# Optimization experiments

Hardware: AMD Instinct MI355X
Metric: run time of the kernel (lower is better)

## Reference

```python
import jax, jax.numpy as jnp
import numpy as np

N, E1, E2, P, H = 4096, 131072, 131072, 65536, 128
ROLE_VOCAB, ROLE_DIM, IDX_VOCAB, IDX_DIM = 8, 16, 1024, 8


def _lin_init(key, fan_in, fan_out):
    k1, k2 = jax.random.split(key)
    bound = 1.0 / np.sqrt(fan_in)
    W = jax.random.uniform(k1, (fan_in, fan_out), jnp.float32, -bound, bound)
    b = jax.random.uniform(k2, (fan_out,), jnp.float32, -bound, bound)
    return W, b


def setup_inputs() -> dict:
    key = jax.random.key(0)
    ks = jax.random.split(key, 24)
    d = {}
    d["block_features"] = jax.random.normal(ks[0], (N, 16), jnp.float32)
    d["role_ids"] = jax.random.randint(ks[1], (N,), 0, ROLE_VOCAB)
    d["b2b_src"] = jax.random.randint(ks[2], (E1,), 0, N)
    d["b2b_dst"] = jax.random.randint(ks[3], (E1,), 0, N)
    d["b2b_w"] = jax.random.uniform(ks[4], (E1,), jnp.float32)
    d["p2b_pin"] = jax.random.randint(ks[5], (E2,), 0, P)
    d["p2b_block"] = jax.random.randint(ks[6], (E2,), 0, N)
    d["p2b_w"] = jax.random.uniform(ks[7], (E2,), jnp.float32)
    d["pins_pos"] = jax.random.normal(ks[8], (P, 2), jnp.float32)
    d["area_targets"] = jax.random.uniform(ks[9], (N,), jnp.float32)
    # parameters
    d["role_emb"] = jax.random.normal(ks[10], (ROLE_VOCAB, ROLE_DIM), jnp.float32)
    d["idx_emb"] = jax.random.normal(ks[11], (IDX_VOCAB, IDX_DIM), jnp.float32)
    d["in_W1"], d["in_b1"] = _lin_init(ks[12], 16 + IDX_DIM + ROLE_DIM, H)
    d["in_W2"], d["in_b2"] = _lin_init(ks[13], H, H)
    d["b2b_W1"], d["b2b_b1"] = _lin_init(ks[14], 2 * H + 1, H)
    d["b2b_W2"], d["b2b_b2"] = _lin_init(ks[15], H, H)
    d["p2b_W1"], d["p2b_b1"] = _lin_init(ks[16], H + 3, H)
    d["p2b_W2"], d["p2b_b2"] = _lin_init(ks[17], H, H)
    d["self_W"], d["self_b"] = _lin_init(ks[18], H, H)
    d["ln_g"] = jnp.ones((H,), jnp.float32)
    d["ln_b"] = jnp.zeros((H,), jnp.float32)
    d["gp_W1"], d["gp_b1"] = _lin_init(ks[19], 2 * H, H)
    d["gp_W2"], d["gp_b2"] = _lin_init(ks[20], H, H)
    return d


def _mlp2(x, W1, b1, W2, b2):
    return jax.nn.relu(x @ W1 + b1) @ W2 + b2


def _forward(block_features, role_ids, b2b_src, b2b_dst, b2b_w, p2b_pin, p2b_block,
             p2b_w, pins_pos, area_targets, role_emb, idx_emb, in_W1, in_b1, in_W2,
             in_b2, b2b_W1, b2b_b1, b2b_W2, b2b_b2, p2b_W1, p2b_b1, p2b_W2, p2b_b2,
             self_W, self_b, ln_g, ln_b, gp_W1, gp_b1, gp_W2, gp_b2):
    n = block_features.shape[0]
    role_e = role_emb[role_ids]                       # [N, role_dim]
    idx_e = idx_emb[jnp.arange(n) % IDX_VOCAB]        # [N, idx_dim]
    x = jnp.concatenate([block_features, role_e, idx_e], axis=-1)
    h = jax.nn.relu(_mlp2(x, in_W1, in_b1, in_W2, in_b2))  # input_proj ends in ReLU

    # --- b2b messages: two directed messages per undirected edge ---
    max_b2b = jax.lax.stop_gradient(jnp.maximum(jnp.max(jnp.abs(b2b_w)), 1.0))
    w = (b2b_w / max_b2b)[:, None]                    # [E1, 1]
    hi, hj = h[b2b_src], h[b2b_dst]                   # [E1, H]
    m_ij = _mlp2(jnp.concatenate([hi, hj, w], -1), b2b_W1, b2b_b1, b2b_W2, b2b_b2)
    m_ji = _mlp2(jnp.concatenate([hj, hi, w], -1), b2b_W1, b2b_b1, b2b_W2, b2b_b2)
    agg = jnp.zeros_like(h).at[b2b_src].add(m_ij).at[b2b_dst].add(m_ji)

    # --- p2b messages ---
    total_area = jnp.maximum(jnp.sum(area_targets), 1e-6)
    case_scale = jax.lax.stop_gradient(jnp.maximum(jnp.sqrt(total_area), 1e-6))
    max_p2b = jax.lax.stop_gradient(jnp.maximum(jnp.max(jnp.abs(p2b_w)), 1.0))
    pin_feats = jnp.concatenate(
        [pins_pos[p2b_pin] / case_scale, (p2b_w / max_p2b)[:, None]], axis=-1)  # [E2, 3]
    m_p = _mlp2(jnp.concatenate([h[p2b_block], pin_feats], -1),
                p2b_W1, p2b_b1, p2b_W2, p2b_b2)
    agg = agg.at[p2b_block].add(m_p)

    # --- combine + LayerNorm ---
    z = h @ self_W + self_b + agg
    mu = jnp.mean(z, axis=-1, keepdims=True)
    var = jnp.mean(jnp.square(z - mu), axis=-1, keepdims=True)
    block_embeddings = (z - mu) / jnp.sqrt(var + 1e-5) * ln_g + ln_b

    pooled = jnp.concatenate(
        [block_embeddings.mean(axis=0), block_embeddings.max(axis=0)], axis=-1)
    graph_embedding = _mlp2(pooled, gp_W1, gp_b1, gp_W2, gp_b2)
    return block_embeddings, graph_embedding


def reference(block_features, role_ids, b2b_src, b2b_dst, b2b_w, p2b_pin, p2b_block,
              p2b_w, pins_pos, area_targets, role_emb, idx_emb, in_W1, in_b1, in_W2,
              in_b2, b2b_W1, b2b_b1, b2b_W2, b2b_b2, p2b_W1, p2b_b1, p2b_W2, p2b_b2,
              self_W, self_b, ln_g, ln_b, gp_W1, gp_b1, gp_W2, gp_b2):
    block_embeddings, graph_embedding = _forward(
        block_features, role_ids, b2b_src, b2b_dst, b2b_w, p2b_pin, p2b_block,
        p2b_w, pins_pos, area_targets, role_emb, idx_emb, in_W1, in_b1, in_W2,
        in_b2, b2b_W1, b2b_b1, b2b_W2, b2b_b2, p2b_W1, p2b_b1, p2b_W2, p2b_b2,
        self_W, self_b, ln_g, ln_b, gp_W1, gp_b1, gp_W2, gp_b2)
    block_mask = jnp.ones((block_features.shape[0],), dtype=bool)
    return block_embeddings, graph_embedding, block_mask
```

## Files before the change

### kernel.cpp

```cpp
#include <hip/hip_runtime.h>
#include <hip/hip_bf16.h>

#define N_NODES 4096
#define HDIM    128
#define E1      131072
#define E2      131072
#define NMSG_B2B (2 * E1)
#define CAPB    192
#define CAPP    96

#define OFF_PSUM   8
#define OFF_PMAX   136
#define OFF_HB     264
#define OFF_P      (OFF_HB + 262144)
#define OFF_Q      (OFF_P + 524288)
#define OFF_R      (OFF_Q + 524288)
#define OFF_CP     (OFF_R + 524288)
#define OFF_B2H    (OFF_CP + 24576)
#define OFF_B2L    (OFF_B2H + 8192)
#define OFF_P2H    (OFF_B2L + 8192)
#define OFF_P2L    (OFF_P2H + 8192)
#define OFF_SWP    (OFF_P2L + 8192)
#define OFF_IW1    (OFF_SWP + 8192)
#define OFF_IW2    (OFF_IW1 + 4096)
#define OFF_WLAST  (OFF_IW2 + 8192)
#define OFF_PEXTRA (OFF_WLAST + 128)
#define OFF_CNTB   (OFF_PEXTRA + 384)
#define OFF_CNTP   (OFF_CNTB + 4096)
#define OFF_BKB    (OFF_CNTP + 4096)
#define OFF_BKP    (OFF_BKB + 2 * N_NODES * CAPB)
#define WS_FLOATS  (OFF_BKP + 2 * N_NODES * CAPP)

typedef short short8 __attribute__((ext_vector_type(8)));
typedef float f32x4 __attribute__((ext_vector_type(4)));

__device__ __forceinline__ unsigned short f2bf(float f) {
  union { float f; unsigned u; } v; v.f = f;
  unsigned r = v.u + 0x7fffu + ((v.u >> 16) & 1u);
  return (unsigned short)(r >> 16);
}
__device__ __forceinline__ float bf2f(unsigned short h) {
  return __uint_as_float((unsigned)h << 16);
}
__device__ __forceinline__ int il(int c) { return ((c & 63) << 1) | (c >> 6); }
__device__ __forceinline__ f32x4 relu4(f32x4 v) {
  f32x4 r;
  r[0] = fmaxf(v[0], 0.f); r[1] = fmaxf(v[1], 0.f);
  r[2] = fmaxf(v[2], 0.f); r[3] = fmaxf(v[3], 0.f);
  return r;
}

__global__ __launch_bounds__(256) void setup_kernel(const float* __restrict__ b2bw,
                                                    const float* __restrict__ p2bw,
                                                    const float* __restrict__ area,
                                                    const float* __restrict__ bW1,
                                                    const float* __restrict__ bW2,
                                                    const float* __restrict__ pW1,
                                                    const float* __restrict__ pW2,
                                                    const float* __restrict__ sWm,
                                                    const float* __restrict__ iW1,
                                                    const float* __restrict__ iW2,
                                                    float* __restrict__ ws) {
  __shared__ float red[256];
  int b = blockIdx.x, t = threadIdx.x;
  if (b < 32) {
    float m = 0.f;
    for (int i = b * 256 + t; i < E1; i += 32 * 256) m = fmaxf(m, fabsf(b2bw[i]));
    red[t] = m; __syncthreads();
    for (int s = 128; s > 0; s >>= 1) { if (t < s) red[t] = fmaxf(red[t], red[t + s]); __syncthreads(); }
    if (t == 0) atomicMax((unsigned*)&ws[0], __float_as_uint(red[0]));
  } else if (b < 64) {
    float m = 0.f;
    for (int i = (b - 32) * 256 + t; i < E2; i += 32 * 256) m = fmaxf(m, fabsf(p2bw[i]));
    red[t] = m; __syncthreads();
    for (int s = 128; s > 0; s >>= 1) { if (t < s) red[t] = fmaxf(red[t], red[t + s]); __syncthreads(); }
    if (t == 0) atomicMax((unsigned*)&ws[1], __float_as_uint(red[0]));
  } else if (b < 96) {
    float s0 = 0.f;
    for (int i = (b - 64) * 256 + t; i < N_NODES; i += 32 * 256) s0 += area[i];
    red[t] = s0; __syncthreads();
    for (int s = 128; s > 0; s >>= 1) { if (t < s) red[t] += red[t + s]; __syncthreads(); }
    if (t == 0) atomicAdd(&ws[2], red[0]);
  } else if (b == 96) {
    if (t < HDIM) ((int*)ws)[OFF_PMAX + t] = 0x80000000;
    int* cB = (int*)ws + OFF_CNTB;
    for (int i = t; i < 2 * N_NODES; i += 256) cB[i] = 0;
  } else {
    unsigned short* Cp  = (unsigned short*)(ws + OFF_CP);
    unsigned short* B2h = (unsigned short*)(ws + OFF_B2H);
    unsigned short* B2l = (unsigned short*)(ws + OFF_B2L);
    unsigned short* P2h = (unsigned short*)(ws + OFF_P2H);
    unsigned short* P2l = (unsigned short*)(ws + OFF_P2L);
    unsigned short* Swp = (unsigned short*)(ws + OFF_SWP);
    unsigned short* I1p = (unsigned short*)(ws + OFF_IW1);
    unsigned short* I2p = (unsigned short*)(ws + OFF_IW2);
    float* wlast = ws + OFF_WLAST;
    float* pextra = ws + OFF_PEXTRA;
    const int total = 156160;
    for (int x = (b - 97) * 256 + t; x < total; x += 128 * 256) {
      if (x < 49152) {
        int j = x & 7, lane = (x >> 3) & 63, ks = (x >> 9) & 3, nc = x >> 11;
        int col = nc * 16 + (lane & 15), k = ks * 32 + (lane >> 4) * 8 + j;
        float v;
        if (col < 128)      v = bW1[k * 128 + col];
        else if (col < 256) v = bW1[(128 + k) * 128 + (col - 128)];
        else                v = pW1[k * 128 + (col - 256)];
        Cp[x] = f2bf(v);
      } else if (x < 114688) {
        int u = (x - 49152) & 16383, which = (x - 49152) >> 14;
        int j = u & 7, lane = (u >> 3) & 63, ks = (u >> 9) & 3, nt = u >> 11;
        int n = nt * 16 + (lane & 15), k = ks * 32 + (lane >> 4) * 8 + j;
        float v = (which < 2) ? bW2[k * 128 + n] : pW2[k * 128 + n];
        unsigned short hi = f2bf(v);
        unsigned short outv = (which & 1) ? f2bf(v - bf2f(hi)) : hi;
        ((which < 2) ? ((which & 1) ? B2l : B2h) : ((which & 1) ? P2l : P2h))[u] = outv;
      } else if (x < 131072) {
        int u = x - 114688;
        int j = u & 7, lane = (u >> 3) & 63, ks = (u >> 9) & 3, nt = u >> 11;
        int n = nt * 16 + (lane & 15), k = ks * 32 + (lane >> 4) * 8 + j;
        Swp[u] = f2bf(sWm[k * 128 + n]);
      } else if (x < 139264) {
        int u = x - 131072;
        int j = u & 7, lane = (u >> 3) & 63, ks = (u >> 9) & 1, nt = u >> 10;
        int n = nt * 16 + (lane & 15), k = ks * 32 + (lane >> 4) * 8 + j;
        I1p[u] = (k < 40) ? f2bf(iW1[k * 128 + n]) : 0;
      } else if (x < 155648) {
        int u = x - 139264;
        int j = u & 7, lane = (u >> 3) & 63, ks = (u >> 9) & 3, nt = u >> 11;
        int n = nt * 16 + (lane & 15), k = ks * 32 + (lane >> 4) * 8 + j;
        I2p[u] = f2bf(iW2[k * 128 + n]);
      } else if (x < 155776) {
        int c = x - 155648;
        wlast[il(c)] = bW1[256 * 128 + c];
      } else {
        int u = x - 155776;
        int r = u >> 7, c = u & 127;
        pextra[r * 128 + il(c)] = pW1[(128 + r) * 128 + c];
      }
    }
  }
}

__global__ __launch_bounds__(512) void mid_kernel(const int* __restrict__ src,
                                                  const int* __restrict__ dst,
                                                  const int* __restrict__ pblk,
                                                  const int* __restrict__ ppin,
                                                  const float* __restrict__ bwv,
                                                  const float* __restrict__ pwv,
                                                  const float* __restrict__ pins,
                                                  const float* __restrict__ bfeat,
                                                  const int* __restrict__ rid,
                                                  const float* __restrict__ remb,
                                                  const float* __restrict__ iemb,
                                                  const float* __restrict__ ib1,
                                                  const float* __restrict__ ib2,
                                                  const float* __restrict__ bb1,
                                                  const float* __restrict__ pb1,
                                                  float* __restrict__ ws,
                                                  unsigned short* __restrict__ hb) {
  __shared__ __attribute__((aligned(16))) unsigned short xs[16 * 72];
  __shared__ __attribute__((aligned(16))) unsigned short h1s[16 * 136];
  __shared__ __attribute__((aligned(16))) unsigned short hs[16 * 136];
  int tid = threadIdx.x;
  if (blockIdx.x < 768) {
    int i = blockIdx.x * 512 + tid;
    int* cntB = (int*)ws + OFF_CNTB;
    int* cntP = (int*)ws + OFF_CNTP;
    uint2* BKB = (uint2*)((int*)ws + OFF_BKB);
    uint2* BKP = (uint2*)((int*)ws + OFF_BKP);
    if (i < NMSG_B2B) {
      int e = i >> 1, d = i & 1;
      int tg = d ? dst[e] : src[e];
      int o  = d ? src[e] : dst[e];
      int pos = atomicAdd(&cntB[tg], 1);
      if (pos < CAPB) {
        uint2 v; v.x = (unsigned)o; v.y = __float_as_uint(bwv[e]);
        BKB[tg * CAPB + pos] = v;
      }
    } else {
      int e = i - NMSG_B2B;
      int pin = ppin[e];
      int tg = pblk[e];
      int pos = atomicAdd(&cntP[tg], 1);
      if (pos < CAPP) {
        uint2 v;
        v.x = ((unsigned)f2bf(pins[pin * 2 + 1]) << 16) | (unsigned)f2bf(pins[pin * 2]);
        v.y = __float_as_uint(pwv[e]);
        BKP[tg * CAPP + pos] = v;
      }
    }
    return;
  }
  const unsigned short* I1p = (const unsigned short*)(ws + OFF_IW1);
  const unsigned short* I2p = (const unsigned short*)(ws + OFF_IW2);
  const unsigned short* Cp  = (const unsigned short*)(ws + OFF_CP);
  float* P = ws + OFF_P;
  float* Q = ws + OFF_Q;
  float* R = ws + OFF_R;
  int n0 = (blockIdx.x - 768) * 16;
  for (int idx = tid; idx < 1024; idx += 512) {
    int m = idx >> 6, c = idx & 63;
    int n = n0 + m;
    float v = 0.f;
    if (c < 16)      v = bfeat[n * 16 + c];
    else if (c < 32) v = remb[rid[n] * 16 + (c - 16)];
    else if (c < 40) v = iemb[(n & 1023) * 8 + (c - 32)];
    xs[m * 72 + c] = f2bf(v);
  }
  __syncthreads();
  int lane = tid & 63, wv = tid >> 6;
  int l15 = lane & 15, q = lane >> 4;
  f32x4 zero = {0.f, 0.f, 0.f, 0.f};
  f32x4 a1 = zero;
#pragma unroll
  for (int ks = 0; ks < 2; ks++) {
    short8 af = *(const short8*)(&xs[l15 * 72 + ks * 32 + q * 8]);
    short8 bfr = *(const short8*)(I1p + ((wv * 2 + ks) * 64 + lane) * 8);
    a1 = __builtin_amdgcn_mfma_f32_16x16x32_bf16(af, bfr, a1, 0, 0, 0);
  }
  {
    int n = wv * 16 + l15;
    float b = ib1[n];
#pragma unroll
    for (int r = 0; r < 4; r++)
      h1s[(q * 4 + r) * 136 + n] = f2bf(fmaxf(a1[r] + b, 0.f));
  }
  __syncthreads();
  f32x4 a2 = zero;
#pragma unroll
  for (int ks = 0; ks < 4; ks++) {
    short8 af = *(const short8*)(&h1s[l15 * 136 + ks * 32 + q * 8]);
    short8 bfr = *(const short8*)(I2p + ((wv * 4 + ks) * 64 + lane) * 8);
    a2 = __builtin_amdgcn_mfma_f32_16x16x32_bf16(af, bfr, a2, 0, 0, 0);
  }
  {
    int n = wv * 16 + l15;
    float b = ib2[n];
#pragma unroll
    for (int r = 0; r < 4; r++) {
      unsigned short hv = f2bf(fmaxf(a2[r] + b, 0.f));
      hs[(q * 4 + r) * 136 + n] = hv;
      hb[(n0 + q * 4 + r) * 128 + n] = hv;
    }
  }
  __syncthreads();
  f32x4 a3[3];
#pragma unroll
  for (int i = 0; i < 3; i++) a3[i] = zero;
#pragma unroll
  for (int ks = 0; ks < 4; ks++) {
    short8 af = *(const short8*)(&hs[l15 * 136 + ks * 32 + q * 8]);
#pragma unroll
    for (int j = 0; j < 3; j++) {
      short8 bfr = *(const short8*)(Cp + (((3 * wv + j) * 4 + ks) * 64 + lane) * 8);
      a3[j] = __builtin_amdgcn_mfma_f32_16x16x32_bf16(af, bfr, a3[j], 0, 0, 0);
    }
  }
#pragma unroll
  for (int j = 0; j < 3; j++) {
    int col = (3 * wv + j) * 16 + l15;
    int arr = col >> 7, cc = col & 127;
    float bias = (arr == 0) ? bb1[cc] : ((arr == 2) ? pb1[cc] : 0.f);
    float* dstp = (arr == 0) ? P : ((arr == 1) ? Q : R);
    int ic = il(cc);
#pragma unroll
    for (int r = 0; r < 4; r++)
      dstp[(n0 + q * 4 + r) * 128 + ic] = a3[j][r] + bias;
  }
}

__global__ __launch_bounds__(1024) void fused_kernel(const unsigned short* __restrict__ hb,
                                                     const float* __restrict__ sb,
                                                     const float* __restrict__ lng,
                                                     const float* __restrict__ lnb,
                                                     const float* __restrict__ bb2,
                                                     const float* __restrict__ pb2,
                                                     const float* __restrict__ gW1,
                                                     const float* __restrict__ gb1,
                                                     const float* __restrict__ gW2,
                                                     const float* __restrict__ gb2,
                                                     float* __restrict__ ws,
                                                     float* __restrict__ out) {
  __shared__ __attribute__((aligned(16))) unsigned short A[16 * 648];
  __shared__ float zp[2][16 * 128];
  __shared__ float zs[16 * 133];
  __shared__ float muS[16], rsg[16];
  __shared__ float partS[16][16], partQ[16][16];
  __shared__ float psumL[8][128];
  __shared__ int   pmaxL[8][128];
  __shared__ int   isLast;
  int tid = threadIdx.x;
  int n0 = blockIdx.x * 16;
  int lane = tid & 63, wv = tid >> 6;
  const int* cntBp = (const int*)ws + OFF_CNTB;
  const int* cntPp = (const int*)ws + OFF_CNTP;
  if (tid < 256) {
    int m = tid >> 4, o = (tid & 15) * 8;
    *(uint4*)(&A[m * 648 + o]) = *(const uint4*)(hb + (n0 + m) * 128 + o);
  }
  {
    const uint2* BKB = (const uint2*)((const int*)ws + OFF_BKB);
    const uint2* BKP = (const uint2*)((const int*)ws + OFF_BKP);
    const float* Pm = ws + OFF_P;
    const float* Qm = ws + OFF_Q;
    const float* Rm = ws + OFF_R;
    float invb = 1.f / fmaxf(__uint_as_float(((const unsigned*)ws)[0]), 1.f);
    float invp = 1.f / fmaxf(__uint_as_float(((const unsigned*)ws)[1]), 1.f);
    float cs = fmaxf(sqrtf(fmaxf(ws[2], 1e-6f)), 1e-6f);
    float invc = 1.f / cs;
    int l5 = lane & 31, hf = lane >> 5;
    f32x4 wl = *(const f32x4*)(ws + OFF_WLAST + 4 * l5);
    f32x4 e0 = *(const f32x4*)(ws + OFF_PEXTRA + 4 * l5);
    f32x4 e1 = *(const f32x4*)(ws + OFF_PEXTRA + 128 + 4 * l5);
    f32x4 e2 = *(const f32x4*)(ws + OFF_PEXTRA + 256 + 4 * l5);
    wl *= invb; e0 *= invc; e1 *= invc; e2 *= invp;
    int ln = wv;
    int node = n0 + ln;
    {
      int cnt = min(cntBp[node], CAPB);
      const uint2* bk = BKB + node * CAPB;
      f32x4 p4 = *(const f32x4*)(Pm + node * 128 + 4 * l5);
      f32x4 acc = {0.f, 0.f, 0.f, 0.f};
      int m = 0;
      if (cnt >= 8) {
        uint2 k0 = bk[hf], k1 = bk[2 + hf], k2 = bk[4 + hf], k3 = bk[6 + hf];
        while (m + 16 <= cnt) {
          uint2 t0 = bk[m + 8 + hf],  t1 = bk[m + 10 + hf];
          uint2 t2 = bk[m + 12 + hf], t3 = bk[m + 14 + hf];
          f32x4 q0 = *(const f32x4*)(Qm + k0.x * 128 + 4 * l5);
          f32x4 q1 = *(const f32x4*)(Qm + k1.x * 128 + 4 * l5);
          f32x4 q2 = *(const f32x4*)(Qm + k2.x * 128 + 4 * l5);
          f32x4 q3 = *(const f32x4*)(Qm + k3.x * 128 + 4 * l5);
          acc += relu4(p4 + __uint_as_float(k0.y) * wl + q0);
          acc += relu4(p4 + __uint_as_float(k1.y) * wl + q1);
          acc += relu4(p4 + __uint_as_float(k2.y) * wl + q2);
          acc += relu4(p4 + __uint_as_float(k3.y) * wl + q3);
          k0 = t0; k1 = t1; k2 = t2; k3 = t3;
          m += 8;
        }
        f32x4 q0 = *(const f32x4*)(Qm + k0.x * 128 + 4 * l5);
        f32x4 q1 = *(const f32x4*)(Qm + k1.x * 128 + 4 * l5);
        f32x4 q2 = *(const f32x4*)(Qm + k2.x * 128 + 4 * l5);
        f32x4 q3 = *(const f32x4*)(Qm + k3.x * 128 + 4 * l5);
        acc += relu4(p4 + __uint_as_float(k0.y) * wl + q0);
        acc += relu4(p4 + __uint_as_float(k1.y) * wl + q1);
        acc += relu4(p4 + __uint_as_float(k2.y) * wl + q2);
        acc += relu4(p4 + __uint_as_float(k3.y) * wl + q3);
        m += 8;
      }
      for (; m + 2 <= cnt; m += 2) {
        uint2 k = bk[m + hf];
        f32x4 q = *(const f32x4*)(Qm + k.x * 128 + 4 * l5);
        acc += relu4(p4 + __uint_as_float(k.y) * wl + q);
      }
      if (m < cnt) {
        uint2 k = bk[m + hf];
        f32x4 q = *(const f32x4*)(Qm + (k.x & (N_NODES - 1)) * 128 + 4 * l5);
        f32x4 v = relu4(p4 + __uint_as_float(k.y) * wl + q);
        if (hf == 0) acc += v;
      }
      f32x4 tot;
#pragma unroll
      for (int j = 0; j < 4; j++) tot[j] = acc[j] + __shfl_xor(acc[j], 32, 64);
      if (hf == 0) {
        unsigned short h0 = f2bf(tot[0]), h1 = f2bf(tot[1]);
        unsigned short h2 = f2bf(tot[2]), h3 = f2bf(tot[3]);
        *(unsigned*)(&A[ln * 648 + 128 + 2 * l5])      = (unsigned)h0 | ((unsigned)h2 << 16);
        *(unsigned*)(&A[ln * 648 + 128 + 64 + 2 * l5]) = (unsigned)h1 | ((unsigned)h3 << 16);
        unsigned short g0 = f2bf(tot[0] - bf2f(h0)), g1 = f2bf(tot[1] - bf2f(h1));
        unsigned short g2 = f2bf(tot[2] - bf2f(h2)), g3 = f2bf(tot[3] - bf2f(h3));
        *(unsigned*)(&A[ln * 648 + 256 + 2 * l5])      = (unsigned)g0 | ((unsigned)g2 << 16);
        *(unsigned*)(&A[ln * 648 + 256 + 64 + 2 * l5]) = (unsigned)g1 | ((unsigned)g3 << 16);
      }
    }
    {
      int cnt = min(cntPp[node], CAPP);
      const uint2* bk = BKP + node * CAPP;
      f32x4 r4 = *(const f32x4*)(Rm + node * 128 + 4 * l5);
      f32x4 acc = {0.f, 0.f, 0.f, 0.f};
      int m = 0;
      for (; m + 4 <= cnt; m += 4) {
        uint2 ka = bk[m + hf], kb = bk[m + 2 + hf];
        float a0 = __uint_as_float((ka.x & 0xFFFFu) << 16);
        float a1 = __uint_as_float(ka.x & 0xFFFF0000u);
        float a2 = __uint_as_float(ka.y);
        float b0 = __uint_as_float((kb.x & 0xFFFFu) << 16);
        float b1 = __uint_as_float(kb.x & 0xFFFF0000u);
        float b2 = __uint_as_float(kb.y);
        acc += relu4(r4 + a0 * e0 + a1 * e1 + a2 * e2);
        acc += relu4(r4 + b0 * e0 + b1 * e1 + b2 * e2);
      }
      for (; m + 2 <= cnt; m += 2) {
        uint2 ka = bk[m + hf];
        float a0 = __uint_as_float((ka.x & 0xFFFFu) << 16);
        float a1 = __uint_as_float(ka.x & 0xFFFF0000u);
        float a2 = __uint_as_float(ka.y);
        acc += relu4(r4 + a0 * e0 + a1 * e1 + a2 * e2);
      }
      if (m < cnt) {
        uint2 ka = bk[m + hf];
        float a0 = __uint_as_float((ka.x & 0xFFFFu) << 16);
        float a1 = __uint_as_float(ka.x & 0xFFFF0000u);
        float a2 = __uint_as_float(ka.y);
        f32x4 v = relu4(r4 + a0 * e0 + a1 * e1 + a2 * e2);
        if (hf == 0) acc += v;
      }
      f32x4 tot;
#pragma unroll
      for (int j = 0; j < 4; j++) tot[j] = acc[j] + __shfl_xor(acc[j], 32, 64);
      if (hf == 0) {
        unsigned short h0 = f2bf(tot[0]), h1 = f2bf(tot[1]);
        unsigned short h2 = f2bf(tot[2]), h3 = f2bf(tot[3]);
        *(unsigned*)(&A[ln * 648 + 384 + 2 * l5])      = (unsigned)h0 | ((unsigned)h2 << 16);
        *(unsigned*)(&A[ln * 648 + 384 + 64 + 2 * l5]) = (unsigned)h1 | ((unsigned)h3 << 16);
        unsigned short g0 = f2bf(tot[0] - bf2f(h0)), g1 = f2bf(tot[1] - bf2f(h1));
        unsigned short g2 = f2bf(tot[2] - bf2f(h2)), g3 = f2bf(tot[3] - bf2f(h3));
        *(unsigned*)(&A[ln * 648 + 512 + 2 * l5])      = (unsigned)g0 | ((unsigned)g2 << 16);
        *(unsigned*)(&A[ln * 648 + 512 + 64 + 2 * l5]) = (unsigned)g1 | ((unsigned)g3 << 16);
      }
    }
  }
  __syncthreads();
  int l15 = lane & 15, q = lane >> 4;
  int ct = wv & 7, half = wv >> 3;
  f32x4 zero = {0.f, 0.f, 0.f, 0.f};
  f32x4 acc = zero;
  const unsigned short* bufs[7] = {
    (const unsigned short*)(ws + OFF_SWP), (const unsigned short*)(ws + OFF_B2H),
    (const unsigned short*)(ws + OFF_B2L), (const unsigned short*)(ws + OFF_B2H),
    (const unsigned short*)(ws + OFF_P2H), (const unsigned short*)(ws + OFF_P2L),
    (const unsigned short*)(ws + OFF_P2H)};
  const int segs[7] = {0, 128, 128, 256, 384, 384, 512};
  int p0 = half ? 4 : 0, p1 = half ? 7 : 4;
  for (int p = p0; p < p1; p++) {
#pragma unroll
    for (int ks = 0; ks < 4; ks++) {
      short8 af = *(const short8*)(&A[l15 * 648 + segs[p] + ks * 32 + q * 8]);
      short8 bfr = *(const short8*)(bufs[p] + ((ct * 4 + ks) * 64 + lane) * 8);
      acc = __builtin_amdgcn_mfma_f32_16x16x32_bf16(af, bfr, acc, 0, 0, 0);
    }
  }
  {
    int nn = ct * 16 + l15;
#pragma unroll
    for (int r = 0; r < 4; r++)
      zp[half][(q * 4 + r) * 128 + nn] = acc[r];
  }
  __syncthreads();
  {
    int idx = tid;
    for (int rep = 0; rep < 2; rep++, idx += 1024) {
      int row = idx >> 7, c = idx & 127;
      float cb = (float)cntBp[n0 + row], cp = (float)cntPp[n0 + row];
      zs[row * 133 + c] = zp[0][row * 128 + c] + zp[1][row * 128 + c]
                        + sb[c] + cb * bb2[c] + cp * pb2[c];
    }
  }
  __syncthreads();
  if (tid < 256) {
    int r = tid >> 4, g = tid & 15;
    const float* zr = &zs[r * 133 + g * 8];
    float s = 0.f, s2 = 0.f;
#pragma unroll
    for (int i = 0; i < 8; i++) { float v = zr[i]; s += v; s2 += v * v; }
    partS[r][g] = s; partQ[r][g] = s2;
  }
  __syncthreads();
  if (tid < 16) {
    float s = 0.f, s2 = 0.f;
#pragma unroll
    for (int g = 0; g < 16; g++) { s += partS[tid][g]; s2 += partQ[tid][g]; }
    float m = s * (1.f / 128.f);
    float var = s2 * (1.f / 128.f) - m * m;
    muS[tid] = m;
    rsg[tid] = rsqrtf(fmaxf(var, 0.f) + 1e-5f);
  }
  __syncthreads();
  {
    int c = tid & 127, grp = tid >> 7;
    float g = lng[c], b = lnb[c];
    float ls = 0.f; int lm = 0x80000000;
    for (int r = grp * 2; r < grp * 2 + 2; r++) {
      float v = (zs[r * 133 + c] - muS[r]) * rsg[r] * g + b;
      out[(n0 + r) * 128 + c] = v;
      ls += v;
      int e = __float_as_int(v);
      e = e >= 0 ? e : (e ^ 0x7fffffff);
      lm = max(lm, e);
    }
    psumL[grp][c] = ls; pmaxL[grp][c] = lm;
  }
  __syncthreads();
  if (tid < 128) {
    float s = 0.f; int mx = 0x80000000;
#pragma unroll
    for (int g = 0; g < 8; g++) { s += psumL[g][tid]; mx = max(mx, pmaxL[g][tid]); }
    atomicAdd(&ws[OFF_PSUM + tid], s);
    atomicMax(&((int*)ws)[OFF_PMAX + tid], mx);
  }
  if (tid < 16) out[N_NODES * HDIM + HDIM + n0 + tid] = 1.0f;
  __syncthreads();
  if (tid == 0) {
    __threadfence();
    int v = atomicAdd(&((int*)ws)[3], 1);
    isLast = (v == (int)gridDim.x - 1);
  }
  __syncthreads();
  if (!isLast) return;
  __shared__ float pooled[256];
  __shared__ float gpart[8][128];
  __shared__ float g1[128];
  if (tid < 128) {
    pooled[tid] = atomicAdd(&ws[OFF_PSUM + tid], 0.f) * (1.f / (float)N_NODES);
  } else if (tid < 256) {
    int e = atomicAdd(&((int*)ws)[OFF_PMAX + (tid - 128)], 0);
    int bits = e >= 0 ? e : (e ^ 0x7fffffff);
    pooled[tid] = __int_as_float(bits);
  }
  __syncthreads();
  {
    int c = tid & 127, g = tid >> 7;
    float acc2 = 0.f;
#pragma unroll 8
    for (int k = g * 32; k < g * 32 + 32; k++) acc2 += pooled[k] * gW1[k * 128 + c];
    gpart[g][c] = acc2;
  }
  __syncthreads();
  if (tid < 128) {
    float s = gb1[tid];
#pragma unroll
    for (int g = 0; g < 8; g++) s += gpart[g][tid];
    g1[tid] = fmaxf(s, 0.f);
  }
  __syncthreads();
  {
    int c = tid & 127, g = tid >> 7;
    float acc2 = 0.f;
#pragma unroll 8
    for (int k = g * 16; k < g * 16 + 16; k++) acc2 += g1[k] * gW2[k * 128 + c];
    gpart[g][c] = acc2;
  }
  __syncthreads();
  if (tid < 128) {
    float s = gb2[tid];
#pragma unroll
    for (int g = 0; g < 8; g++) s += gpart[g][tid];
    out[N_NODES * HDIM + tid] = s;
  }
}

extern "C" void kernel_launch(void* const* d_in, const int* in_sizes, int n_in,
                              void* d_out, int out_size, void* d_ws, size_t ws_size,
                              hipStream_t stream) {
  const float* bfeat = (const float*)d_in[0];
  const int*   rid   = (const int*)d_in[1];
  const int*   bsrc  = (const int*)d_in[2];
  const int*   bdst  = (const int*)d_in[3];
  const float* bw    = (const float*)d_in[4];
  const int*   ppin  = (const int*)d_in[5];
  const int*   pblk  = (const int*)d_in[6];
  const float* pw    = (const float*)d_in[7];
  const float* pins  = (const float*)d_in[8];
  const float* area  = (const float*)d_in[9];
  const float* remb  = (const float*)d_in[10];
  const float* iemb  = (const float*)d_in[11];
  const float* inW1  = (const float*)d_in[12];
  const float* inb1  = (const float*)d_in[13];
  const float* inW2  = (const float*)d_in[14];
  const float* inb2  = (const float*)d_in[15];
  const float* bW1   = (const float*)d_in[16];
  const float* bb1   = (const float*)d_in[17];
  const float* bW2   = (const float*)d_in[18];
  const float* bb2   = (const float*)d_in[19];
  const float* pW1   = (const float*)d_in[20];
  const float* pb1   = (const float*)d_in[21];
  const float* pW2   = (const float*)d_in[22];
  const float* pb2   = (const float*)d_in[23];
  const float* sW    = (const float*)d_in[24];
  const float* sb    = (const float*)d_in[25];
  const float* lng   = (const float*)d_in[26];
  const float* lnb   = (const float*)d_in[27];
  const float* gW1   = (const float*)d_in[28];
  const float* gb1   = (const float*)d_in[29];
  const float* gW2   = (const float*)d_in[30];
  const float* gb2   = (const float*)d_in[31];

  float* ws  = (float*)d_ws;
  float* out = (float*)d_out;
  unsigned short* hb = (unsigned short*)(ws + OFF_HB);

  hipMemsetAsync(d_ws, 0, 264 * sizeof(float), stream);
  setup_kernel<<<225, 256, 0, stream>>>(bw, pw, area,
                                        bW1, bW2, pW1, pW2, sW, inW1, inW2, ws);
  mid_kernel<<<1024, 512, 0, stream>>>(bsrc, bdst, pblk, ppin, bw, pw, pins,
                                       bfeat, rid, remb, iemb, inb1, inb2, bb1, pb1,
                                       ws, hb);
  fused_kernel<<<256, 1024, 0, stream>>>(hb, sb, lng, lnb, bb2, pb2,
                                         gW1, gb1, gW2, gb2, ws, out);
}
```

Before: 191.0 us.

## Move edge bucketing into setup kernel and stage bucket entries in shared memory

The edge bucketing (atomic slot claim and write of edge records into per-node buckets) moves from mid_kernel into setup_kernel, so mid_kernel runs only the node MLP on 256 blocks. The fused kernel now copies the first STGB/STGP bucket entries per node into shared memory, reusing the z-buffer space through a union, and reads any overflow from global memory. The global atomic reductions for the weight maxima and the area sum become per-block partials that the fused kernel reduces with shuffles. This trades a larger setup launch and an extra staging pass for less global latency in the gather loops and fewer atomics.

```diff
diff --git a/kernel.cpp b/kernel.cpp
--- a/kernel.cpp
+++ b/kernel.cpp
@@ -8,10 +8,15 @@
 #define NMSG_B2B (2 * E1)
 #define CAPB    192
 #define CAPP    96
-
-#define OFF_PSUM   8
-#define OFF_PMAX   136
-#define OFF_HB     264
+#define STGB    96
+#define STGP    48
+
+#define OFF_CNTB   8
+#define OFF_CNTP   (OFF_CNTB + 4096)
+#define OFF_RED    (OFF_CNTP + 4096)
+#define OFF_PSUM   (OFF_RED + 96)
+#define OFF_PMAX   (OFF_PSUM + 128)
+#define OFF_HB     (OFF_PMAX + 128)
 #define OFF_P      (OFF_HB + 262144)
 #define OFF_Q      (OFF_P + 524288)
 #define OFF_R      (OFF_Q + 524288)
@@ -25,9 +30,7 @@
 #define OFF_IW2    (OFF_IW1 + 4096)
 #define OFF_WLAST  (OFF_IW2 + 8192)
 #define OFF_PEXTRA (OFF_WLAST + 128)
-#define OFF_CNTB   (OFF_PEXTRA + 384)
-#define OFF_CNTP   (OFF_CNTB + 4096)
-#define OFF_BKB    (OFF_CNTP + 4096)
+#define OFF_BKB    (OFF_PEXTRA + 384)
 #define OFF_BKP    (OFF_BKB + 2 * N_NODES * CAPB)
 #define WS_FLOATS  (OFF_BKP + 2 * N_NODES * CAPP)
 
@@ -60,6 +63,11 @@
                                                     const float* __restrict__ sWm,
                                                     const float* __restrict__ iW1,
                                                     const float* __restrict__ iW2,
+                                                    const int* __restrict__ src,
+                                                    const int* __restrict__ dst,
+                                                    const int* __restrict__ pblk,
+                                                    const int* __restrict__ ppin,
+                                                    const float* __restrict__ pins,
                                                     float* __restrict__ ws) {
   __shared__ float red[256];
   int b = blockIdx.x, t = threadIdx.x;
@@ -68,24 +76,25 @@
     for (int i = b * 256 + t; i < E1; i += 32 * 256) m = fmaxf(m, fabsf(b2bw[i]));
     red[t] = m; __syncthreads();
     for (int s = 128; s > 0; s >>= 1) { if (t < s) red[t] = fmaxf(red[t], red[t + s]); __syncthreads(); }
-    if (t == 0) atomicMax((unsigned*)&ws[0], __float_as_uint(red[0]));
+    if (t == 0) ws[OFF_RED + b] = red[0];
   } else if (b < 64) {
     float m = 0.f;
     for (int i = (b - 32) * 256 + t; i < E2; i += 32 * 256) m = fmaxf(m, fabsf(p2bw[i]));
     red[t] = m; __syncthreads();
     for (int s = 128; s > 0; s >>= 1) { if (t < s) red[t] = fmaxf(red[t], red[t + s]); __syncthreads(); }
-    if (t == 0) atomicMax((unsigned*)&ws[1], __float_as_uint(red[0]));
+    if (t == 0) ws[OFF_RED + b] = red[0];
   } else if (b < 96) {
     float s0 = 0.f;
     for (int i = (b - 64) * 256 + t; i < N_NODES; i += 32 * 256) s0 += area[i];
     red[t] = s0; __syncthreads();
     for (int s = 128; s > 0; s >>= 1) { if (t < s) red[t] += red[t + s]; __syncthreads(); }
-    if (t == 0) atomicAdd(&ws[2], red[0]);
+    if (t == 0) ws[OFF_RED + b] = red[0];
   } else if (b == 96) {
-    if (t < HDIM) ((int*)ws)[OFF_PMAX + t] = 0x80000000;
-    int* cB = (int*)ws + OFF_CNTB;
-    for (int i = t; i < 2 * N_NODES; i += 256) cB[i] = 0;
-  } else {
+    if (t < HDIM) {
+      ws[OFF_PSUM + t] = 0.f;
+      ((int*)ws)[OFF_PMAX + t] = 0x80000000;
+    }
+  } else if (b < 225) {
     unsigned short* Cp  = (unsigned short*)(ws + OFF_CP);
     unsigned short* B2h = (unsigned short*)(ws + OFF_B2H);
     unsigned short* B2l = (unsigned short*)(ws + OFF_B2L);
@@ -138,17 +147,37 @@
         pextra[r * 128 + il(c)] = pW1[(128 + r) * 128 + c];
       }
     }
+  } else {
+    int i = (b - 225) * 256 + t;
+    int* cntB = (int*)ws + OFF_CNTB;
+    int* cntP = (int*)ws + OFF_CNTP;
+    uint2* BKB = (uint2*)((int*)ws + OFF_BKB);
+    uint2* BKP = (uint2*)((int*)ws + OFF_BKP);
+    if (i < NMSG_B2B) {
+      int e = i >> 1, d = i & 1;
+      int tg = d ? dst[e] : src[e];
+      int o  = d ? src[e] : dst[e];
+      int pos = atomicAdd(&cntB[tg], 1);
+      if (pos < CAPB) {
+        uint2 v; v.x = (unsigned)o; v.y = __float_as_uint(b2bw[e]);
+        BKB[tg * CAPB + pos] = v;
+      }
+    } else {
+      int e = i - NMSG_B2B;
+      int pin = ppin[e];
+      int tg = pblk[e];
+      int pos = atomicAdd(&cntP[tg], 1);
+      if (pos < CAPP) {
+        uint2 v;
+        v.x = ((unsigned)f2bf(pins[pin * 2 + 1]) << 16) | (unsigned)f2bf(pins[pin * 2]);
+        v.y = __float_as_uint(p2bw[e]);
+        BKP[tg * CAPP + pos] = v;
+      }
+    }
   }
 }
 
-__global__ __launch_bounds__(512) void mid_kernel(const int* __restrict__ src,
-                                                  const int* __restrict__ dst,
-                                                  const int* __restrict__ pblk,
-                                                  const int* __restrict__ ppin,
-                                                  const float* __restrict__ bwv,
-                                                  const float* __restrict__ pwv,
-                                                  const float* __restrict__ pins,
-                                                  const float* __restrict__ bfeat,
+__global__ __launch_bounds__(512) void mid_kernel(const float* __restrict__ bfeat,
                                                   const int* __restrict__ rid,
                                                   const float* __restrict__ remb,
                                                   const float* __restrict__ iemb,
@@ -162,42 +191,13 @@
   __shared__ __attribute__((aligned(16))) unsigned short h1s[16 * 136];
   __shared__ __attribute__((aligned(16))) unsigned short hs[16 * 136];
   int tid = threadIdx.x;
-  if (blockIdx.x < 768) {
-    int i = blockIdx.x * 512 + tid;
-    int* cntB = (int*)ws + OFF_CNTB;
-    int* cntP = (int*)ws + OFF_CNTP;
-    uint2* BKB = (uint2*)((int*)ws + OFF_BKB);
-    uint2* BKP = (uint2*)((int*)ws + OFF_BKP);
-    if (i < NMSG_B2B) {
-      int e = i >> 1, d = i & 1;
-      int tg = d ? dst[e] : src[e];
-      int o  = d ? src[e] : dst[e];
-      int pos = atomicAdd(&cntB[tg], 1);
-      if (pos < CAPB) {
-        uint2 v; v.x = (unsigned)o; v.y = __float_as_uint(bwv[e]);
-        BKB[tg * CAPB + pos] = v;
-      }
-    } else {
-      int e = i - NMSG_B2B;
-      int pin = ppin[e];
-      int tg = pblk[e];
-      int pos = atomicAdd(&cntP[tg], 1);
-      if (pos < CAPP) {
-        uint2 v;
-        v.x = ((unsigned)f2bf(pins[pin * 2 + 1]) << 16) | (unsigned)f2bf(pins[pin * 2]);
-        v.y = __float_as_uint(pwv[e]);
-        BKP[tg * CAPP + pos] = v;
-      }
-    }
-    return;
-  }
   const unsigned short* I1p = (const unsigned short*)(ws + OFF_IW1);
   const unsigned short* I2p = (const unsigned short*)(ws + OFF_IW2);
   const unsigned short* Cp  = (const unsigned short*)(ws + OFF_CP);
   float* P = ws + OFF_P;
   float* Q = ws + OFF_Q;
   float* R = ws + OFF_R;
-  int n0 = (blockIdx.x - 768) * 16;
+  int n0 = blockIdx.x * 16;
   for (int idx = tid; idx < 1024; idx += 512) {
     int m = idx >> 6, c = idx & 63;
     int n = n0 + m;
@@ -282,62 +282,76 @@
                                                      float* __restrict__ ws,
                                                      float* __restrict__ out) {
   __shared__ __attribute__((aligned(16))) unsigned short A[16 * 648];
-  __shared__ float zp[2][16 * 128];
-  __shared__ float zs[16 * 133];
+  __shared__ __attribute__((aligned(16))) union {
+    struct { float zp[2][16 * 128]; float zs[16 * 133]; } t;
+    struct { uint2 bkb[16][STGB]; uint2 bkp[16][STGP]; } e;
+  } U;
   __shared__ float muS[16], rsg[16];
   __shared__ float partS[16][16], partQ[16][16];
   __shared__ float psumL[8][128];
   __shared__ int   pmaxL[8][128];
+  __shared__ float sInvB, sInvP, sInvC;
   __shared__ int   isLast;
   int tid = threadIdx.x;
   int n0 = blockIdx.x * 16;
   int lane = tid & 63, wv = tid >> 6;
   const int* cntBp = (const int*)ws + OFF_CNTB;
   const int* cntPp = (const int*)ws + OFF_CNTP;
+  const uint2* BKB = (const uint2*)((const int*)ws + OFF_BKB);
+  const uint2* BKP = (const uint2*)((const int*)ws + OFF_BKP);
   if (tid < 256) {
     int m = tid >> 4, o = (tid & 15) * 8;
     *(uint4*)(&A[m * 648 + o]) = *(const uint4*)(hb + (n0 + m) * 128 + o);
   }
-  {
-    const uint2* BKB = (const uint2*)((const int*)ws + OFF_BKB);
-    const uint2* BKP = (const uint2*)((const int*)ws + OFF_BKP);
+  for (int idx = tid; idx < 16 * STGB; idx += 1024) {
+    int m = idx / STGB, j = idx - m * STGB;
+    if (j < cntBp[n0 + m]) U.e.bkb[m][j] = BKB[(n0 + m) * CAPB + j];
+  }
+  for (int idx = tid; idx < 16 * STGP; idx += 1024) {
+    int m = idx / STGP, j = idx - m * STGP;
+    if (j < cntPp[n0 + m]) U.e.bkp[m][j] = BKP[(n0 + m) * CAPP + j];
+  }
+  if (tid < 96) {
+    float v = ws[OFF_RED + tid];
+    if (tid < 64) {
+#pragma unroll
+      for (int s = 1; s < 32; s <<= 1) v = fmaxf(v, __shfl_xor(v, s, 64));
+      if (tid == 0)  sInvB = 1.f / fmaxf(v, 1.f);
+      if (tid == 32) sInvP = 1.f / fmaxf(v, 1.f);
+    } else {
+#pragma unroll
+      for (int s = 1; s < 32; s <<= 1) v += __shfl_xor(v, s, 64);
+      if (tid == 64) {
+        float cs = fmaxf(sqrtf(fmaxf(v, 1e-6f)), 1e-6f);
+        sInvC = 1.f / cs;
+      }
+    }
+  }
+  int l5 = lane & 31, hf = lane >> 5;
+  f32x4 wl = *(const f32x4*)(ws + OFF_WLAST + 4 * l5);
+  f32x4 e0 = *(const f32x4*)(ws + OFF_PEXTRA + 4 * l5);
+  f32x4 e1 = *(const f32x4*)(ws + OFF_PEXTRA + 128 + 4 * l5);
+  f32x4 e2 = *(const f32x4*)(ws + OFF_PEXTRA + 256 + 4 * l5);
+  __syncthreads();
+  {
     const float* Pm = ws + OFF_P;
     const float* Qm = ws + OFF_Q;
     const float* Rm = ws + OFF_R;
-    float invb = 1.f / fmaxf(__uint_as_float(((const unsigned*)ws)[0]), 1.f);
-    float invp = 1.f / fmaxf(__uint_as_float(((const unsigned*)ws)[1]), 1.f);
-    float cs = fmaxf(sqrtf(fmaxf(ws[2], 1e-6f)), 1e-6f);
-    float invc = 1.f / cs;
-    int l5 = lane & 31, hf = lane >> 5;
-    f32x4 wl = *(const f32x4*)(ws + OFF_WLAST + 4 * l5);
-    f32x4 e0 = *(const f32x4*)(ws + OFF_PEXTRA + 4 * l5);
-    f32x4 e1 = *(const f32x4*)(ws + OFF_PEXTRA + 128 + 4 * l5);
-    f32x4 e2 = *(const f32x4*)(ws + OFF_PEXTRA + 256 + 4 * l5);
+    float invb = sInvB, invp = sInvP, invc = sInvC;
     wl *= invb; e0 *= invc; e1 *= invc; e2 *= invp;
     int ln = wv;
     int node = n0 + ln;
     {
       int cnt = min(cntBp[node], CAPB);
-      const uint2* bk = BKB + node * CAPB;
+      int stg = min(cnt, STGB);
+      const uint2* bkL = U.e.bkb[ln];
+      const uint2* bkG = BKB + node * CAPB;
       f32x4 p4 = *(const f32x4*)(Pm + node * 128 + 4 * l5);
       f32x4 acc = {0.f, 0.f, 0.f, 0.f};
       int m = 0;
-      if (cnt >= 8) {
-        uint2 k0 = bk[hf], k1 = bk[2 + hf], k2 = bk[4 + hf], k3 = bk[6 + hf];
-        while (m + 16 <= cnt) {
-          uint2 t0 = bk[m + 8 + hf],  t1 = bk[m + 10 + hf];
-          uint2 t2 = bk[m + 12 + hf], t3 = bk[m + 14 + hf];
-          f32x4 q0 = *(const f32x4*)(Qm + k0.x * 128 + 4 * l5);
-          f32x4 q1 = *(const f32x4*)(Qm + k1.x * 128 + 4 * l5);
-          f32x4 q2 = *(const f32x4*)(Qm + k2.x * 128 + 4 * l5);
-          f32x4 q3 = *(const f32x4*)(Qm + k3.x * 128 + 4 * l5);
-          acc += relu4(p4 + __uint_as_float(k0.y) * wl + q0);
-          acc += relu4(p4 + __uint_as_float(k1.y) * wl + q1);
-          acc += relu4(p4 + __uint_as_float(k2.y) * wl + q2);
-          acc += relu4(p4 + __uint_as_float(k3.y) * wl + q3);
-          k0 = t0; k1 = t1; k2 = t2; k3 = t3;
-          m += 8;
-        }
+      for (; m + 8 <= stg; m += 8) {
+        uint2 k0 = bkL[m + hf], k1 = bkL[m + 2 + hf];
+        uint2 k2 = bkL[m + 4 + hf], k3 = bkL[m + 6 + hf];
         f32x4 q0 = *(const f32x4*)(Qm + k0.x * 128 + 4 * l5);
         f32x4 q1 = *(const f32x4*)(Qm + k1.x * 128 + 4 * l5);
         f32x4 q2 = *(const f32x4*)(Qm + k2.x * 128 + 4 * l5);
@@ -346,15 +360,26 @@
         acc += relu4(p4 + __uint_as_float(k1.y) * wl + q1);
         acc += relu4(p4 + __uint_as_float(k2.y) * wl + q2);
         acc += relu4(p4 + __uint_as_float(k3.y) * wl + q3);
-        m += 8;
-      }
-      for (; m + 2 <= cnt; m += 2) {
-        uint2 k = bk[m + hf];
+      }
+      for (; m + 2 <= stg; m += 2) {
+        uint2 k = bkL[m + hf];
         f32x4 q = *(const f32x4*)(Qm + k.x * 128 + 4 * l5);
         acc += relu4(p4 + __uint_as_float(k.y) * wl + q);
       }
+      if (m < stg) {
+        uint2 k = bkL[m + hf];
+        f32x4 q = *(const f32x4*)(Qm + (k.x & (N_NODES - 1)) * 128 + 4 * l5);
+        f32x4 v = relu4(p4 + __uint_as_float(k.y) * wl + q);
+        if (hf == 0) acc += v;
+        m++;
+      }
+      for (; m + 2 <= cnt; m += 2) {
+        uint2 k = bkG[m + hf];
+        f32x4 q = *(const f32x4*)(Qm + k.x * 128 + 4 * l5);
+        acc += relu4(p4 + __uint_as_float(k.y) * wl + q);
+      }
       if (m < cnt) {
-        uint2 k = bk[m + hf];
+        uint2 k = bkG[m + hf];
         f32x4 q = *(const f32x4*)(Qm + (k.x & (N_NODES - 1)) * 128 + 4 * l5);
         f32x4 v = relu4(p4 + __uint_as_float(k.y) * wl + q);
         if (hf == 0) acc += v;
@@ -375,12 +400,14 @@
     }
     {
       int cnt = min(cntPp[node], CAPP);
-      const uint2* bk = BKP + node * CAPP;
+      int stg = min(cnt, STGP);
+      const uint2* bkL = U.e.bkp[ln];
+      const uint2* bkG = BKP + node * CAPP;
       f32x4 r4 = *(const f32x4*)(Rm + node * 128 + 4 * l5);
       f32x4 acc = {0.f, 0.f, 0.f, 0.f};
       int m = 0;
-      for (; m + 4 <= cnt; m += 4) {
-        uint2 ka = bk[m + hf], kb = bk[m + 2 + hf];
+      for (; m + 4 <= stg; m += 4) {
+        uint2 ka = bkL[m + hf], kb = bkL[m + 2 + hf];
         float a0 = __uint_as_float((ka.x & 0xFFFFu) << 16);
         float a1 = __uint_as_float(ka.x & 0xFFFF0000u);
         float a2 = __uint_as_float(ka.y);
@@ -390,15 +417,31 @@
         acc += relu4(r4 + a0 * e0 + a1 * e1 + a2 * e2);
         acc += relu4(r4 + b0 * e0 + b1 * e1 + b2 * e2);
       }
-      for (; m + 2 <= cnt; m += 2) {
-        uint2 ka = bk[m + hf];
+      for (; m + 2 <= stg; m += 2) {
+        uint2 ka = bkL[m + hf];
         float a0 = __uint_as_float((ka.x & 0xFFFFu) << 16);
         float a1 = __uint_as_float(ka.x & 0xFFFF0000u);
         float a2 = __uint_as_float(ka.y);
         acc += relu4(r4 + a0 * e0 + a1 * e1 + a2 * e2);
       }
+      if (m < stg) {
+        uint2 ka = bkL[m + hf];
+        float a0 = __uint_as_float((ka.x & 0xFFFFu) << 16);
+        float a1 = __uint_as_float(ka.x & 0xFFFF0000u);
+        float a2 = __uint_as_float(ka.y);
+        f32x4 v = relu4(r4 + a0 * e0 + a1 * e1 + a2 * e2);
+        if (hf == 0) acc += v;
+        m++;
+      }
+      for (; m + 2 <= cnt; m += 2) {
+        uint2 ka = bkG[m + hf];
+        float a0 = __uint_as_float((ka.x & 0xFFFFu) << 16);
+        float a1 = __uint_as_float(ka.x & 0xFFFF0000u);
+        float a2 = __uint_as_float(ka.y);
+        acc += relu4(r4 + a0 * e0 + a1 * e1 + a2 * e2);
+      }
       if (m < cnt) {
-        uint2 ka = bk[m + hf];
+        uint2 ka = bkG[m + hf];
         float a0 = __uint_as_float((ka.x & 0xFFFFu) << 16);
         float a1 = __uint_as_float(ka.x & 0xFFFF0000u);
         float a2 = __uint_as_float(ka.y);
@@ -444,7 +487,7 @@
     int nn = ct * 16 + l15;
 #pragma unroll
     for (int r = 0; r < 4; r++)
-      zp[half][(q * 4 + r) * 128 + nn] = acc[r];
+      U.t.zp[half][(q * 4 + r) * 128 + nn] = acc[r];
   }
   __syncthreads();
   {
@@ -452,14 +495,14 @@
     for (int rep = 0; rep < 2; rep++, idx += 1024) {
       int row = idx >> 7, c = idx & 127;
       float cb = (float)cntBp[n0 + row], cp = (float)cntPp[n0 + row];
-      zs[row * 133 + c] = zp[0][row * 128 + c] + zp[1][row * 128 + c]
-                        + sb[c] + cb * bb2[c] + cp * pb2[c];
+      U.t.zs[row * 133 + c] = U.t.zp[0][row * 128 + c] + U.t.zp[1][row * 128 + c]
+                            + sb[c] + cb * bb2[c] + cp * pb2[c];
     }
   }
   __syncthreads();
   if (tid < 256) {
     int r = tid >> 4, g = tid & 15;
-    const float* zr = &zs[r * 133 + g * 8];
+    const float* zr = &U.t.zs[r * 133 + g * 8];
     float s = 0.f, s2 = 0.f;
 #pragma unroll
     for (int i = 0; i < 8; i++) { float v = zr[i]; s += v; s2 += v * v; }
@@ -481,7 +524,7 @@
     float g = lng[c], b = lnb[c];
     float ls = 0.f; int lm = 0x80000000;
     for (int r = grp * 2; r < grp * 2 + 2; r++) {
-      float v = (zs[r * 133 + c] - muS[r]) * rsg[r] * g + b;
+      float v = (U.t.zs[r * 133 + c] - muS[r]) * rsg[r] * g + b;
       out[(n0 + r) * 128 + c] = v;
       ls += v;
       int e = __float_as_int(v);
@@ -589,12 +632,12 @@
   float* out = (float*)d_out;
   unsigned short* hb = (unsigned short*)(ws + OFF_HB);
 
-  hipMemsetAsync(d_ws, 0, 264 * sizeof(float), stream);
-  setup_kernel<<<225, 256, 0, stream>>>(bw, pw, area,
-                                        bW1, bW2, pW1, pW2, sW, inW1, inW2, ws);
-  mid_kernel<<<1024, 512, 0, stream>>>(bsrc, bdst, pblk, ppin, bw, pw, pins,
-                                       bfeat, rid, remb, iemb, inb1, inb2, bb1, pb1,
-                                       ws, hb);
+  hipMemsetAsync(d_ws, 0, OFF_RED * sizeof(float), stream);
+  setup_kernel<<<1761, 256, 0, stream>>>(bw, pw, area,
+                                         bW1, bW2, pW1, pW2, sW, inW1, inW2,
+                                         bsrc, bdst, pblk, ppin, pins, ws);
+  mid_kernel<<<256, 512, 0, stream>>>(bfeat, rid, remb, iemb, inb1, inb2, bb1, pb1,
+                                      ws, hb);
   fused_kernel<<<256, 1024, 0, stream>>>(hb, sb, lng, lnb, bb2, pb2,
                                          gW1, gb1, gW2, gb2, ws, out);
 }
```

New measurement: 190.0 us. No clear change (-0.5%).
